# Kernel tuning notes

Hardware: AMD Instinct MI355X
Metric: run time of the kernel (lower is better)

## Reference

```python
import jax, jax.numpy as jnp
import numpy as np

B, N, E = 8, 10000, 320000   # graphs, nodes per graph, edges per graph
C_IN, C_OUT = 128, 128


def setup_inputs() -> dict:
    key = jax.random.key(0)
    k_x, k_w, k_b, k_r, k_c, k_n = jax.random.split(key, 6)
    x = jax.random.normal(k_x, (B, N, C_IN), dtype=jnp.float32)
    weight = jax.random.normal(k_w, (C_IN, C_OUT), dtype=jnp.float32)
    bias = jax.random.normal(k_b, (C_OUT,), dtype=jnp.float32)
    edge_row = jax.random.randint(k_r, (B, E), 0, N, dtype=jnp.int32)
    edge_col = jax.random.randint(k_c, (B, E), 0, N, dtype=jnp.int32)
    edge_val = jnp.ones((B, E), dtype=jnp.float32)
    num_nodes = jax.random.randint(k_n, (B,), 1, N, dtype=jnp.int32)
    return {"x": x, "weight": weight, "bias": bias,
            "edge_row": edge_row, "edge_col": edge_col, "edge_val": edge_val,
            "num_nodes": num_nodes}


def reference(x, weight, bias, edge_row, edge_col, edge_val, num_nodes):
    # x: [B, N, C_in] -> linear transform
    h = jnp.einsum('bnc,co->bno', x, weight) + bias          # [B, N, C_out]

    def spmm_one(rows, cols, vals, h_b):
        # A @ h_b for one graph via gather + segment-sum scatter
        msgs = vals[:, None] * h_b[cols]                      # [E, C_out]
        agg = jax.ops.segment_sum(msgs, rows, num_segments=N) # [N, C_out]
        deg = jax.ops.segment_sum(vals, rows, num_segments=N) # row sums of A
        return agg / jnp.clip(deg, 1.0)[:, None]              # clamp(min=1)

    out = jax.vmap(spmm_one)(edge_row, edge_col, edge_val, h)  # [B, N, C_out]

    # zero out padded nodes: out[i, num_nodes[i]:, :] = 0
    mask = jnp.arange(N)[None, :] < num_nodes[:, None]         # [B, N]
    return out * mask[:, :, None].astype(out.dtype)
```

## Files before the change

### kernel.cpp

```cpp
#include <hip/hip_runtime.h>

#define BG   8
#define NN   10000
#define EE   320000
#define CC   128
#define BN   (BG*NN)
#define BE   (BG*EE)

#define NBKT   157
#define BROWS  64
#define CAP    2560
#define CHUNK  4096
#define BPG    ((EE + CHUNK - 1) / CHUNK)


__global__ __launch_bounds__(256) void k_bin(const int* __restrict__ edge_row,
                                             const int* __restrict__ edge_col,
                                             const float* __restrict__ edge_val,
                                             int* __restrict__ cursor,
                                             int2* __restrict__ binned) {
    int g = blockIdx.x / BPG;
    int cstart = (blockIdx.x % BPG) * CHUNK;
    int t = threadIdx.x;
    __shared__ int lh[NBKT];
    __shared__ int lbase[NBKT];
    for (int i = t; i < NBKT; i += 256) lh[i] = 0;
    __syncthreads();
    int rows[CHUNK / 256];
#pragma unroll
    for (int j = 0; j < CHUNK / 256; j++) {
        int e = cstart + j * 256 + t;
        if (e < EE) {
            int r = edge_row[(size_t)g * EE + e];
            rows[j] = r;
            atomicAdd(&lh[r >> 6], 1);
        } else rows[j] = -1;
    }
    __syncthreads();
    for (int i = t; i < NBKT; i += 256) {
        int c = lh[i];
        lbase[i] = c ? atomicAdd(&cursor[g * NBKT + i], c) : 0;
        lh[i] = 0;
    }
    __syncthreads();
#pragma unroll
    for (int j = 0; j < CHUNK / 256; j++) {
        if (rows[j] >= 0) {
            int e = cstart + j * 256 + t;
            int r = rows[j];
            int bkt = r >> 6;
            int pos = lbase[bkt] + atomicAdd(&lh[bkt], 1);
            binned[((size_t)g * NBKT + bkt) * CAP + pos] =
                make_int2(((r & 63) << 14) | edge_col[(size_t)g * EE + e],
                          __float_as_int(edge_val[(size_t)g * EE + e]));
        }
    }
}

__global__ __launch_bounds__(256) void k_sort(const int2* __restrict__ binned,
                                              const int* __restrict__ bcnt,
                                              int2* __restrict__ sorted,
                                              int* __restrict__ row_off,
                                              int* __restrict__ row_cnt,
                                              float* __restrict__ deg) {
    int g = blockIdx.x / NBKT;
    int bkt = blockIdx.x % NBKT;
    int t = threadIdx.x;
    __shared__ int2 ein[CAP];
    __shared__ int2 eout[CAP];
    __shared__ int cnts[BROWS], excl[BROWS], curs[BROWS];
    __shared__ float degl[BROWS];
    if (t < BROWS) { cnts[t] = 0; degl[t] = 0.f; }
    __syncthreads();
    int cnt = bcnt[g * NBKT + bkt];
    if (cnt > CAP) cnt = CAP;
    const int2* src = binned + ((size_t)g * NBKT + bkt) * CAP;
    for (int i = t; i < cnt; i += 256) {
        int2 ed = src[i];
        ein[i] = ed;
        atomicAdd(&cnts[ed.x >> 14], 1);
        atomicAdd(&degl[ed.x >> 14], __int_as_float(ed.y));
    }
    __syncthreads();
    if (t < 64) {
        int own = cnts[t];
        int v = own;
#pragma unroll
        for (int d = 1; d < 64; d <<= 1) {
            int n = __shfl_up(v, d);
            if (t >= d) v += n;
        }
        excl[t] = v - own;
        curs[t] = v - own;
        int gr = bkt * BROWS + t;
        if (gr < NN) {
            int row = g * NN + gr;
            row_off[row] = bkt * CAP + (v - own);
            row_cnt[row] = own;
            deg[row] = degl[t];
        }
    }
    __syncthreads();
    for (int i = t; i < cnt; i += 256) {
        int2 ed = ein[i];
        int pos = atomicAdd(&curs[ed.x >> 14], 1);
        eout[pos] = make_int2(ed.x & 0x3FFF, ed.y);
    }
    __syncthreads();
    int2* dst = sorted + ((size_t)g * NBKT + bkt) * CAP;
    for (int i = t; i < cnt; i += 256) dst[i] = eout[i];
}

__global__ __launch_bounds__(256) void k_gather(const float* __restrict__ x,
                                                const int* __restrict__ row_off,
                                                const int* __restrict__ row_cnt,
                                                const int2* __restrict__ sorted,
                                                float* __restrict__ aggx,
                                                int pass) {
    int bid = blockIdx.x;
    int g = bid & 7;
    int chunk = bid >> 3;
    int wid = threadIdx.x >> 6, lane = threadIdx.x & 63;
    int r = chunk * 4 + wid;
    int bn = g * NN + r;
    int start = __builtin_amdgcn_readfirstlane(row_off[bn]);
    int cnt = __builtin_amdgcn_readfirstlane(row_cnt[bn]);
    const float* xb = x + (size_t)g * NN * CC + pass * 64 + lane;
    const long long* ep =
        (const long long*)(sorted + (size_t)g * NBKT * CAP + start);

    float a0 = 0.f, a1 = 0.f;
    int e = 0;
    for (; e + 8 <= cnt; e += 8) {
        int c[8]; float v[8];
#pragma unroll
        for (int j = 0; j < 8; j++) {
            long long m = __builtin_nontemporal_load(ep + e + j);
            c[j] = __builtin_amdgcn_readfirstlane((int)m);
            v[j] = __int_as_float(__builtin_amdgcn_readfirstlane((int)(m >> 32)));
        }
        float xv[8];
#pragma unroll
        for (int j = 0; j < 8; j++)
            xv[j] = xb[(size_t)c[j] << 7];
#pragma unroll
        for (int j = 0; j < 8; j++) {
            if (j & 1) a1 += v[j] * xv[j];
            else       a0 += v[j] * xv[j];
        }
    }
    for (; e < cnt; e++) {
        long long m = __builtin_nontemporal_load(ep + e);
        int c0 = __builtin_amdgcn_readfirstlane((int)m);
        float v0 = __int_as_float(__builtin_amdgcn_readfirstlane((int)(m >> 32)));
        a0 += v0 * xb[(size_t)c0 << 7];
    }
    __builtin_nontemporal_store(a0 + a1,
                                aggx + (size_t)bn * CC + pass * 64 + lane);
}

__global__ __launch_bounds__(256) void k_gemm(float* __restrict__ io,
                                              const float* __restrict__ W,
                                              const float* __restrict__ bias,
                                              const float* __restrict__ deg,
                                              const int* __restrict__ num_nodes) {
    __shared__ float at[64][132];
    int t = threadIdx.x;
    int row0 = blockIdx.x * 64;

    const float4* src = (const float4*)(io + (size_t)row0 * CC);
#pragma unroll
    for (int i = 0; i < 8; i++) {
        int f4 = t + i * 256;
        float4 v = src[f4];
        int row = f4 >> 5;
        int col4 = f4 & 31;
        *(float4*)(&at[row][col4 * 4]) = v;
    }
    __syncthreads();

    int cg = t & 15;
    int rg = t >> 4;
    float acc[4][8] = {};
#pragma unroll 4
    for (int k = 0; k < 128; k++) {
        float4 w0 = *(const float4*)(W + k * 128 + cg * 8);
        float4 w1 = *(const float4*)(W + k * 128 + cg * 8 + 4);
        float a0 = at[rg * 4 + 0][k];
        float a1 = at[rg * 4 + 1][k];
        float a2 = at[rg * 4 + 2][k];
        float a3 = at[rg * 4 + 3][k];
        acc[0][0] += a0 * w0.x; acc[0][1] += a0 * w0.y; acc[0][2] += a0 * w0.z; acc[0][3] += a0 * w0.w;
        acc[0][4] += a0 * w1.x; acc[0][5] += a0 * w1.y; acc[0][6] += a0 * w1.z; acc[0][7] += a0 * w1.w;
        acc[1][0] += a1 * w0.x; acc[1][1] += a1 * w0.y; acc[1][2] += a1 * w0.z; acc[1][3] += a1 * w0.w;
        acc[1][4] += a1 * w1.x; acc[1][5] += a1 * w1.y; acc[1][6] += a1 * w1.z; acc[1][7] += a1 * w1.w;
        acc[2][0] += a2 * w0.x; acc[2][1] += a2 * w0.y; acc[2][2] += a2 * w0.z; acc[2][3] += a2 * w0.w;
        acc[2][4] += a2 * w1.x; acc[2][5] += a2 * w1.y; acc[2][6] += a2 * w1.z; acc[2][7] += a2 * w1.w;
        acc[3][0] += a3 * w0.x; acc[3][1] += a3 * w0.y; acc[3][2] += a3 * w0.z; acc[3][3] += a3 * w0.w;
        acc[3][4] += a3 * w1.x; acc[3][5] += a3 * w1.y; acc[3][6] += a3 * w1.z; acc[3][7] += a3 * w1.w;
    }

    float4 b0 = *(const float4*)(bias + cg * 8);
    float4 b1 = *(const float4*)(bias + cg * 8 + 4);
    float bb[8] = { b0.x, b0.y, b0.z, b0.w, b1.x, b1.y, b1.z, b1.w };

#pragma unroll
    for (int i = 0; i < 4; i++) {
        int grow = row0 + rg * 4 + i;
        int b = grow / NN;
        int r = grow - b * NN;
        float d = deg[grow];
        float sc = 1.0f / fmaxf(d, 1.0f);
        bool alive = r < num_nodes[b];
        float o[8];
#pragma unroll
        for (int j = 0; j < 8; j++)
            o[j] = alive ? (acc[i][j] + d * bb[j]) * sc : 0.0f;
        float* dst = io + (size_t)grow * CC + cg * 8;
        *(float4*)(dst)     = make_float4(o[0], o[1], o[2], o[3]);
        *(float4*)(dst + 4) = make_float4(o[4], o[5], o[6], o[7]);
    }
}

extern "C" void kernel_launch(void* const* d_in, const int* in_sizes, int n_in,
                              void* d_out, int out_size, void* d_ws, size_t ws_size,
                              hipStream_t stream) {
    const float* x        = (const float*)d_in[0];
    const float* weight   = (const float*)d_in[1];
    const float* bias     = (const float*)d_in[2];
    const int*   edge_row = (const int*)d_in[3];
    const int*   edge_col = (const int*)d_in[4];
    const float* edge_val = (const float*)d_in[5];
    const int*   num_nodes= (const int*)d_in[6];
    float* out = (float*)d_out;

    int2*  binned  = (int2*)d_out;
    int2*  sorted  = (int2*)d_ws;
    float* deg     = (float*)(sorted + (size_t)BG * NBKT * CAP);
    int*   row_off = (int*)(deg + BN);
    int*   row_cnt = row_off + BN;
    int*   cursor  = row_cnt + BN;

    hipMemsetAsync(cursor, 0, BG * NBKT * sizeof(int), stream);
    k_bin<<<BG * BPG, 256, 0, stream>>>(edge_row, edge_col, edge_val, cursor, binned);
    k_sort<<<BG * NBKT, 256, 0, stream>>>(binned, cursor, sorted,
                                          row_off, row_cnt, deg);
    k_gather<<<8 * (NN / 4), 256, 0, stream>>>(x, row_off, row_cnt, sorted, out, 0);
    k_gather<<<8 * (NN / 4), 256, 0, stream>>>(x, row_off, row_cnt, sorted, out, 1);
    k_gemm<<<BN / 64, 256, 0, stream>>>(out, weight, bias, deg, num_nodes);
}
```

Before: 305.0 us.

## Stage weight matrix in LDS and stream activation rows from global in GEMM

The GEMM kernel now loads the full 128x128 weight matrix into shared memory (64 KB) instead of staging a 64-row activation tile. Each thread reads float4 chunks of its four activation rows straight from global memory, while weights come from LDS. The goal is to cut repeated global/L1 weight reads per k step and use wider vector activation loads. In exchange, LDS use rises to 64 KB per block, which may limit occupancy, and the per-thread activation loads are strided across rows rather than coalesced.

```diff
diff --git a/kernel.cpp b/kernel.cpp
--- a/kernel.cpp
+++ b/kernel.cpp
@@ -164,40 +164,46 @@
                                               const float* __restrict__ bias,
                                               const float* __restrict__ deg,
                                               const int* __restrict__ num_nodes) {
-    __shared__ float at[64][132];
+    __shared__ float4 wl[128 * 32];
     int t = threadIdx.x;
+    const float4* Wv = (const float4*)W;
+#pragma unroll
+    for (int i = 0; i < 16; i++) wl[t + i * 256] = Wv[t + i * 256];
+    __syncthreads();
+
     int row0 = blockIdx.x * 64;
-
-    const float4* src = (const float4*)(io + (size_t)row0 * CC);
-#pragma unroll
-    for (int i = 0; i < 8; i++) {
-        int f4 = t + i * 256;
-        float4 v = src[f4];
-        int row = f4 >> 5;
-        int col4 = f4 & 31;
-        *(float4*)(&at[row][col4 * 4]) = v;
-    }
-    __syncthreads();
-
     int cg = t & 15;
     int rg = t >> 4;
+    const float* a0p = io + (size_t)(row0 + rg * 4 + 0) * CC;
+    const float* a1p = io + (size_t)(row0 + rg * 4 + 1) * CC;
+    const float* a2p = io + (size_t)(row0 + rg * 4 + 2) * CC;
+    const float* a3p = io + (size_t)(row0 + rg * 4 + 3) * CC;
+
     float acc[4][8] = {};
-#pragma unroll 4
-    for (int k = 0; k < 128; k++) {
-        float4 w0 = *(const float4*)(W + k * 128 + cg * 8);
-        float4 w1 = *(const float4*)(W + k * 128 + cg * 8 + 4);
-        float a0 = at[rg * 4 + 0][k];
-        float a1 = at[rg * 4 + 1][k];
-        float a2 = at[rg * 4 + 2][k];
-        float a3 = at[rg * 4 + 3][k];
-        acc[0][0] += a0 * w0.x; acc[0][1] += a0 * w0.y; acc[0][2] += a0 * w0.z; acc[0][3] += a0 * w0.w;
-        acc[0][4] += a0 * w1.x; acc[0][5] += a0 * w1.y; acc[0][6] += a0 * w1.z; acc[0][7] += a0 * w1.w;
-        acc[1][0] += a1 * w0.x; acc[1][1] += a1 * w0.y; acc[1][2] += a1 * w0.z; acc[1][3] += a1 * w0.w;
-        acc[1][4] += a1 * w1.x; acc[1][5] += a1 * w1.y; acc[1][6] += a1 * w1.z; acc[1][7] += a1 * w1.w;
-        acc[2][0] += a2 * w0.x; acc[2][1] += a2 * w0.y; acc[2][2] += a2 * w0.z; acc[2][3] += a2 * w0.w;
-        acc[2][4] += a2 * w1.x; acc[2][5] += a2 * w1.y; acc[2][6] += a2 * w1.z; acc[2][7] += a2 * w1.w;
-        acc[3][0] += a3 * w0.x; acc[3][1] += a3 * w0.y; acc[3][2] += a3 * w0.z; acc[3][3] += a3 * w0.w;
-        acc[3][4] += a3 * w1.x; acc[3][5] += a3 * w1.y; acc[3][6] += a3 * w1.z; acc[3][7] += a3 * w1.w;
+#pragma unroll 2
+    for (int kc = 0; kc < 128; kc += 4) {
+        float4 a[4];
+        a[0] = *(const float4*)(a0p + kc);
+        a[1] = *(const float4*)(a1p + kc);
+        a[2] = *(const float4*)(a2p + kc);
+        a[3] = *(const float4*)(a3p + kc);
+#pragma unroll
+        for (int kk = 0; kk < 4; kk++) {
+            float4 w0 = wl[(kc + kk) * 32 + cg * 2];
+            float4 w1 = wl[(kc + kk) * 32 + cg * 2 + 1];
+            float av[4];
+            av[0] = (kk == 0) ? a[0].x : (kk == 1) ? a[0].y : (kk == 2) ? a[0].z : a[0].w;
+            av[1] = (kk == 0) ? a[1].x : (kk == 1) ? a[1].y : (kk == 2) ? a[1].z : a[1].w;
+            av[2] = (kk == 0) ? a[2].x : (kk == 1) ? a[2].y : (kk == 2) ? a[2].z : a[2].w;
+            av[3] = (kk == 0) ? a[3].x : (kk == 1) ? a[3].y : (kk == 2) ? a[3].z : a[3].w;
+#pragma unroll
+            for (int i = 0; i < 4; i++) {
+                acc[i][0] += av[i] * w0.x; acc[i][1] += av[i] * w0.y;
+                acc[i][2] += av[i] * w0.z; acc[i][3] += av[i] * w0.w;
+                acc[i][4] += av[i] * w1.x; acc[i][5] += av[i] * w1.y;
+                acc[i][6] += av[i] * w1.z; acc[i][7] += av[i] * w1.w;
+            }
+        }
     }
 
     float4 b0 = *(const float4*)(bias + cg * 8);
```

Measured after the change: 295.6 us. 3.1% less time.
